# Performance work log

Measured on AMD Instinct MI355X. Metric: run time of the kernel, lower is better.

Reference implementation:

```python
import jax, jax.numpy as jnp
import numpy as np

N = 40000      # num nodes
E = 640000     # num edges (avg degree 16)
D = 128        # hidden_size
L = 2          # num_gcn


def setup_inputs() -> dict:
    key = jax.random.key(0)
    k1, k2, k3, k4, k5, k6 = jax.random.split(key, 6)
    h = jax.random.normal(k1, (N, D), dtype=jnp.float32)
    edge_src = jax.random.randint(k2, (E,), 0, N, dtype=jnp.int32)
    edge_dst = jax.random.randint(k3, (E,), 0, N, dtype=jnp.int32)
    w_self = jax.random.uniform(k4, (E,), dtype=jnp.float32)
    w_ppi = jax.random.uniform(k5, (E,), dtype=jnp.float32)
    # Xavier-uniform linear weights, zero bias (matches reset_parameters)
    limit = float(np.sqrt(6.0 / (D + D)))
    W = jax.random.uniform(k6, (L, D, D), dtype=jnp.float32, minval=-limit, maxval=limit)
    b = jnp.zeros((L, D), dtype=jnp.float32)
    return {"h": h, "edge_src": edge_src, "edge_dst": edge_dst,
            "w_self": w_self, "w_ppi": w_ppi, "W": W, "b": b}


def _agg(h, src, dst, w):
    # edge-weighted SpMM: sum over incoming edges of w_e * h[src_e]
    msgs = h[src] * w[:, None]                       # [E, D]
    return jax.ops.segment_sum(msgs, dst, num_segments=N)  # [N, D]


def reference(h, edge_src, edge_dst, w_self, w_ppi, W, b):
    for l in range(L):
        res = _agg(h, edge_src, edge_dst, w_self)        # residual aggregation
        ppi = _agg(h, edge_src, edge_dst, w_ppi)         # ppi aggregation
        # NodeUpdate: dropout(relu(linear(ppi))) + res  (dropout=0 -> identity)
        h = jax.nn.relu(ppi @ W[l].T + b[l]) + res
    return h
```

## Files before the change

### kernel.cpp

```cpp
#include <hip/hip_runtime.h>

#define D 128
#define TILE 16
#define CAP 64

typedef _Float16 f16x2 __attribute__((ext_vector_type(2)));
typedef _Float16 f16x8 __attribute__((ext_vector_type(8)));
typedef float f32x4  __attribute__((ext_vector_type(4)));

static __device__ __forceinline__ unsigned pk2h(float a, float b) {
    auto h = __builtin_amdgcn_cvt_pkrtz(a, b);
    return __builtin_bit_cast(unsigned, h);
}

__global__ __launch_bounds__(256) void cvt2z_kernel(const float4* __restrict__ a,
                                                    uint2* __restrict__ oa, int n4a,
                                                    const float4* __restrict__ bsrc,
                                                    uint2* __restrict__ ob, int n4b,
                                                    int4* __restrict__ zbuf, int nz4) {
    int i = blockIdx.x * 256 + threadIdx.x;
    if (i < n4a) {
        float4 v = a[i];
        uint2 o;
        o.x = pk2h(v.x, v.y);
        o.y = pk2h(v.z, v.w);
        oa[i] = o;
    }
    int j = i - n4a;
    if (j >= 0 && j < n4b) {
        float4 v = bsrc[j];
        uint2 o;
        o.x = pk2h(v.x, v.y);
        o.y = pk2h(v.z, v.w);
        ob[j] = o;
    }
    int k = j - n4b;
    if (k >= 0 && k < nz4) zbuf[k] = make_int4(0, 0, 0, 0);
}

__global__ __launch_bounds__(256) void build_kernel(const int* __restrict__ src,
                                                    const int* __restrict__ dst,
                                                    const float* __restrict__ wself,
                                                    const float* __restrict__ wppi,
                                                    int* __restrict__ cnt,
                                                    uint2* __restrict__ edges, int E) {
    int i = blockIdx.x * 256 + threadIdx.x;
    if (i < E) {
        int d = dst[i];
        int r = atomicAdd(&cnt[d], 1);
        if (r < CAP) {
            uint2 e;
            e.x = (unsigned)src[i];
            e.y = pk2h(wself[i], wppi[i]);
            edges[(d << 6) + r] = e;
        }
    }
}

static __device__ __forceinline__ void edge_fma(unsigned wbits, uint4 hv,
                                                f16x2 (&ra)[4], f16x2 (&pa)[4]) {
    f16x2 wv = __builtin_bit_cast(f16x2, wbits);
    f16x2 wa = {wv.x, wv.x};
    f16x2 wb = {wv.y, wv.y};
    f16x2 h01 = __builtin_bit_cast(f16x2, hv.x);
    f16x2 h23 = __builtin_bit_cast(f16x2, hv.y);
    f16x2 h45 = __builtin_bit_cast(f16x2, hv.z);
    f16x2 h67 = __builtin_bit_cast(f16x2, hv.w);
    ra[0] = __builtin_elementwise_fma(wa, h01, ra[0]);
    ra[1] = __builtin_elementwise_fma(wa, h23, ra[1]);
    ra[2] = __builtin_elementwise_fma(wa, h45, ra[2]);
    ra[3] = __builtin_elementwise_fma(wa, h67, ra[3]);
    pa[0] = __builtin_elementwise_fma(wb, h01, pa[0]);
    pa[1] = __builtin_elementwise_fma(wb, h23, pa[1]);
    pa[2] = __builtin_elementwise_fma(wb, h45, pa[2]);
    pa[3] = __builtin_elementwise_fma(wb, h67, pa[3]);
}

static __device__ __forceinline__ void agg_node(const unsigned short* __restrict__ h16,
                                                const uint2* __restrict__ edges,
                                                const uint2 (&er)[8], int cn, int beg,
                                                int q, int c8, int nn,
                                                f16x2 (&ra)[4], f16x2 (&pa)[4]) {
    int ng = (cn + 3) >> 2;
    if (ng > 8) ng = 8;
    unsigned s[8], wz[8];
    #pragma unroll
    for (int j = 0; j < 8; ++j) {
        int slot = 4 * j + q;
        bool act = slot < cn;
        unsigned sj = act ? er[j].x : er[0].x;
        s[j]  = sj < (unsigned)nn ? sj : 0u;
        wz[j] = act ? er[j].y : 0u;
    }
    uint4 hv[8];
    #pragma unroll
    for (int j = 0; j < 8; ++j)
        if (j < ng)
            hv[j] = *(const uint4*)(h16 + (size_t)s[j] * D + c8 * 8);
    #pragma unroll
    for (int j = 0; j < 8; ++j)
        if (j < ng)
            edge_fma(wz[j], hv[j], ra, pa);
    if (cn > 32) {
        int end = beg + cn;
        for (int e = beg + 32; e < end; e += 16) {
            uint2 err[4]; unsigned wzz[4];
            #pragma unroll
            for (int j = 0; j < 4; ++j) {
                int idx = e + 4 * j + q;
                bool act = idx < end;
                err[j] = edges[act ? idx : beg];
                wzz[j] = act ? err[j].y : 0u;
            }
            uint4 hh[4];
            #pragma unroll
            for (int j = 0; j < 4; ++j) {
                unsigned sj = err[j].x < (unsigned)nn ? err[j].x : 0u;
                hh[j] = *(const uint4*)(h16 + (size_t)sj * D + c8 * 8);
            }
            #pragma unroll
            for (int j = 0; j < 4; ++j) edge_fma(wzz[j], hh[j], ra, pa);
        }
    }
}

static __device__ __forceinline__ unsigned red2(unsigned x) {
    f16x2 a = __builtin_bit_cast(f16x2, x);
    unsigned u = (unsigned)__shfl_xor((int)x, 16, 64);
    a = a + __builtin_bit_cast(f16x2, u);
    unsigned u2 = (unsigned)__shfl_xor((int)__builtin_bit_cast(unsigned, a), 32, 64);
    a = a + __builtin_bit_cast(f16x2, u2);
    return __builtin_bit_cast(unsigned, a);
}

__global__ __launch_bounds__(1024, 2) void layer_kernel(const unsigned short* __restrict__ h16,
                                                        const int* __restrict__ cnt,
                                                        const uint2* __restrict__ edges,
                                                        const unsigned short* __restrict__ Wb,
                                                        const float* __restrict__ bias,
                                                        float* __restrict__ out,
                                                        unsigned short* __restrict__ out16,
                                                        int n) {
    __shared__ unsigned short ppi_lds[TILE][136];
    __shared__ float          res_lds[TILE][132];
    int t = threadIdx.x;
    int w = t >> 6, lane = t & 63;
    int tile = blockIdx.x;
    int q  = lane >> 4;
    int c8 = lane & 15;

    int m16 = lane & 15, quad = lane >> 4;
    f16x8 bfr[4] = {};
    float bb = 0.f;
    if (w < 8) {
        const _Float16* brow = (const _Float16*)Wb + (size_t)(w * 16 + m16) * D + quad * 8;
        #pragma unroll
        for (int kt = 0; kt < 4; ++kt) bfr[kt] = *(const f16x8*)(brow + kt * 32);
        bb = bias[w * 16 + m16];
    }

    int node = tile * TILE + w;
    int beg = node << 6;
    int cn = cnt[node];
    uint2 er[8];
    #pragma unroll
    for (int j = 0; j < 8; ++j) er[j] = edges[beg + 4 * j + q];

    int c = cn < CAP ? cn : CAP;
    f16x2 ra[4] = {};
    f16x2 pa[4] = {};
    agg_node(h16, edges, er, c, beg, q, c8, n, ra, pa);

    unsigned v[8];
    #pragma unroll
    for (int i = 0; i < 4; ++i) v[i]     = red2(__builtin_bit_cast(unsigned, ra[i]));
    #pragma unroll
    for (int i = 0; i < 4; ++i) v[i + 4] = red2(__builtin_bit_cast(unsigned, pa[i]));

    if (q == 0) {
        f16x2 r01 = __builtin_bit_cast(f16x2, v[0]);
        f16x2 r23 = __builtin_bit_cast(f16x2, v[1]);
        f16x2 r45 = __builtin_bit_cast(f16x2, v[2]);
        f16x2 r67 = __builtin_bit_cast(f16x2, v[3]);
        *(float4*)&res_lds[w][c8 * 8]     = make_float4((float)r01.x, (float)r01.y,
                                                        (float)r23.x, (float)r23.y);
        *(float4*)&res_lds[w][c8 * 8 + 4] = make_float4((float)r45.x, (float)r45.y,
                                                        (float)r67.x, (float)r67.y);
        uint4 o = make_uint4(v[4], v[5], v[6], v[7]);
        *(uint4*)&ppi_lds[w][c8 * 8] = o;
    }
    __syncthreads();

    if (w < 8) {
        f16x8 a[4];
        const _Float16* arow = (const _Float16*)&ppi_lds[m16][quad * 8];
        #pragma unroll
        for (int kt = 0; kt < 4; ++kt) a[kt] = *(const f16x8*)(arow + kt * 32);

        f32x4 acc = {0.f, 0.f, 0.f, 0.f};
        #pragma unroll
        for (int kt = 0; kt < 4; ++kt)
            acc = __builtin_amdgcn_mfma_f32_16x16x32_f16(a[kt], bfr[kt], acc, 0, 0, 0);

        int o = w * 16 + m16;
        #pragma unroll
        for (int r = 0; r < 4; ++r) {
            int nd = quad * 4 + r;
            float vv = fmaxf(acc[r] + bb, 0.f) + res_lds[nd][o];
            size_t gi = (size_t)(tile * TILE + nd) * D + o;
            if (out)   out[gi] = vv;
            if (out16) {
                _Float16 hvv = (_Float16)vv;
                out16[gi] = __builtin_bit_cast(unsigned short, hvv);
            }
        }
    }
}

extern "C" void kernel_launch(void* const* d_in, const int* in_sizes, int n_in,
                              void* d_out, int out_size, void* d_ws, size_t ws_size,
                              hipStream_t stream) {
    const float* h0    = (const float*)d_in[0];
    const int*   esrc  = (const int*)d_in[1];
    const int*   edst  = (const int*)d_in[2];
    const float* wself = (const float*)d_in[3];
    const float* wppi  = (const float*)d_in[4];
    const float* W     = (const float*)d_in[5];
    const float* b     = (const float*)d_in[6];
    float*       out   = (float*)d_out;

    const int N = in_sizes[0] / D;
    const int E = in_sizes[1];
    const int L = in_sizes[5] / (D * D);

    char* ws = (char*)d_ws;
    unsigned short* h16a  = (unsigned short*)ws; ws += (size_t)N * D * 2;
    unsigned short* h16b  = (unsigned short*)ws; ws += (size_t)N * D * 2;
    uint2*          edges = (uint2*)ws;          ws += (size_t)N * CAP * 8;
    unsigned short* Wb    = (unsigned short*)ws; ws += (size_t)L * D * D * 2;
    int* cnt = (int*)ws;  ws += (size_t)N * 4;

    int n4h = N * D / 4;
    int n4w = L * D * D / 4;
    int nz4 = N / 4;
    int tot = n4h + n4w + nz4;
    cvt2z_kernel<<<(tot + 255) / 256, 256, 0, stream>>>(
        (const float4*)h0, (uint2*)h16a, n4h,
        (const float4*)W, (uint2*)Wb, n4w,
        (int4*)cnt, nz4);

    int eb = (E + 255) / 256;
    build_kernel<<<eb, 256, 0, stream>>>(esrc, edst, wself, wppi, cnt, edges, E);

    int ntiles = N / TILE;
    layer_kernel<<<ntiles, 1024, 0, stream>>>(h16a, cnt, edges, Wb, b,
                                              (L > 1) ? nullptr : out,
                                              (L > 1) ? h16b : nullptr, N);
    for (int l = 1; l < L; ++l) {
        bool last = (l + 1 == L);
        layer_kernel<<<ntiles, 1024, 0, stream>>>(h16b, cnt, edges,
                                                  Wb + (size_t)l * D * D, b + (size_t)l * D,
                                                  last ? out : nullptr,
                                                  last ? nullptr : h16a, N);
        unsigned short* tmp = h16a; h16a = h16b; h16b = tmp;
    }
}
```

Before: 199.2 us.

## Halve layer block to 512 threads, two nodes per wave, zero-fill edge slots

The layer kernel now uses 512-thread blocks where each wave aggregates two nodes sequentially, so all 8 waves take part in the MFMA linear step and none sit idle. The edge bucket array is zero-filled in the conversion kernel. Padded slots then carry zero weight and src 0, which removes the per-slot masking and index clamping in the gather. The cost is an extra write of the whole edge buffer (N*64*8 bytes) on every call, traded for simpler gather code and higher occupancy.

```diff
diff --git a/kernel.cpp b/kernel.cpp
--- a/kernel.cpp
+++ b/kernel.cpp
@@ -17,7 +17,8 @@
                                                     uint2* __restrict__ oa, int n4a,
                                                     const float4* __restrict__ bsrc,
                                                     uint2* __restrict__ ob, int n4b,
-                                                    int4* __restrict__ zbuf, int nz4) {
+                                                    int4* __restrict__ z1, int nz1,
+                                                    int4* __restrict__ z2, int nz2) {
     int i = blockIdx.x * 256 + threadIdx.x;
     if (i < n4a) {
         float4 v = a[i];
@@ -35,7 +36,9 @@
         ob[j] = o;
     }
     int k = j - n4b;
-    if (k >= 0 && k < nz4) zbuf[k] = make_int4(0, 0, 0, 0);
+    if (k >= 0 && k < nz1) z1[k] = make_int4(0, 0, 0, 0);
+    int m = k - nz1;
+    if (m >= 0 && m < nz2) z2[m] = make_int4(0, 0, 0, 0);
 }
 
 __global__ __launch_bounds__(256) void build_kernel(const int* __restrict__ src,
@@ -76,54 +79,6 @@
     pa[3] = __builtin_elementwise_fma(wb, h67, pa[3]);
 }
 
-static __device__ __forceinline__ void agg_node(const unsigned short* __restrict__ h16,
-                                                const uint2* __restrict__ edges,
-                                                const uint2 (&er)[8], int cn, int beg,
-                                                int q, int c8, int nn,
-                                                f16x2 (&ra)[4], f16x2 (&pa)[4]) {
-    int ng = (cn + 3) >> 2;
-    if (ng > 8) ng = 8;
-    unsigned s[8], wz[8];
-    #pragma unroll
-    for (int j = 0; j < 8; ++j) {
-        int slot = 4 * j + q;
-        bool act = slot < cn;
-        unsigned sj = act ? er[j].x : er[0].x;
-        s[j]  = sj < (unsigned)nn ? sj : 0u;
-        wz[j] = act ? er[j].y : 0u;
-    }
-    uint4 hv[8];
-    #pragma unroll
-    for (int j = 0; j < 8; ++j)
-        if (j < ng)
-            hv[j] = *(const uint4*)(h16 + (size_t)s[j] * D + c8 * 8);
-    #pragma unroll
-    for (int j = 0; j < 8; ++j)
-        if (j < ng)
-            edge_fma(wz[j], hv[j], ra, pa);
-    if (cn > 32) {
-        int end = beg + cn;
-        for (int e = beg + 32; e < end; e += 16) {
-            uint2 err[4]; unsigned wzz[4];
-            #pragma unroll
-            for (int j = 0; j < 4; ++j) {
-                int idx = e + 4 * j + q;
-                bool act = idx < end;
-                err[j] = edges[act ? idx : beg];
-                wzz[j] = act ? err[j].y : 0u;
-            }
-            uint4 hh[4];
-            #pragma unroll
-            for (int j = 0; j < 4; ++j) {
-                unsigned sj = err[j].x < (unsigned)nn ? err[j].x : 0u;
-                hh[j] = *(const uint4*)(h16 + (size_t)sj * D + c8 * 8);
-            }
-            #pragma unroll
-            for (int j = 0; j < 4; ++j) edge_fma(wzz[j], hh[j], ra, pa);
-        }
-    }
-}
-
 static __device__ __forceinline__ unsigned red2(unsigned x) {
     f16x2 a = __builtin_bit_cast(f16x2, x);
     unsigned u = (unsigned)__shfl_xor((int)x, 16, 64);
@@ -133,14 +88,14 @@
     return __builtin_bit_cast(unsigned, a);
 }
 
-__global__ __launch_bounds__(1024, 2) void layer_kernel(const unsigned short* __restrict__ h16,
-                                                        const int* __restrict__ cnt,
-                                                        const uint2* __restrict__ edges,
-                                                        const unsigned short* __restrict__ Wb,
-                                                        const float* __restrict__ bias,
-                                                        float* __restrict__ out,
-                                                        unsigned short* __restrict__ out16,
-                                                        int n) {
+__global__ __launch_bounds__(512, 6) void layer_kernel(const unsigned short* __restrict__ h16,
+                                                       const int* __restrict__ cnt,
+                                                       const uint2* __restrict__ edges,
+                                                       const unsigned short* __restrict__ Wb,
+                                                       const float* __restrict__ bias,
+                                                       float* __restrict__ out,
+                                                       unsigned short* __restrict__ out16,
+                                                       int n) {
     __shared__ unsigned short ppi_lds[TILE][136];
     __shared__ float          res_lds[TILE][132];
     int t = threadIdx.x;
@@ -149,53 +104,75 @@
     int q  = lane >> 4;
     int c8 = lane & 15;
 
-    int m16 = lane & 15, quad = lane >> 4;
-    f16x8 bfr[4] = {};
-    float bb = 0.f;
-    if (w < 8) {
-        const _Float16* brow = (const _Float16*)Wb + (size_t)(w * 16 + m16) * D + quad * 8;
-        #pragma unroll
-        for (int kt = 0; kt < 4; ++kt) bfr[kt] = *(const f16x8*)(brow + kt * 32);
-        bb = bias[w * 16 + m16];
-    }
-
-    int node = tile * TILE + w;
-    int beg = node << 6;
-    int cn = cnt[node];
-    uint2 er[8];
     #pragma unroll
-    for (int j = 0; j < 8; ++j) er[j] = edges[beg + 4 * j + q];
-
-    int c = cn < CAP ? cn : CAP;
-    f16x2 ra[4] = {};
-    f16x2 pa[4] = {};
-    agg_node(h16, edges, er, c, beg, q, c8, n, ra, pa);
-
-    unsigned v[8];
-    #pragma unroll
-    for (int i = 0; i < 4; ++i) v[i]     = red2(__builtin_bit_cast(unsigned, ra[i]));
-    #pragma unroll
-    for (int i = 0; i < 4; ++i) v[i + 4] = red2(__builtin_bit_cast(unsigned, pa[i]));
-
-    if (q == 0) {
-        f16x2 r01 = __builtin_bit_cast(f16x2, v[0]);
-        f16x2 r23 = __builtin_bit_cast(f16x2, v[1]);
-        f16x2 r45 = __builtin_bit_cast(f16x2, v[2]);
-        f16x2 r67 = __builtin_bit_cast(f16x2, v[3]);
-        *(float4*)&res_lds[w][c8 * 8]     = make_float4((float)r01.x, (float)r01.y,
-                                                        (float)r23.x, (float)r23.y);
-        *(float4*)&res_lds[w][c8 * 8 + 4] = make_float4((float)r45.x, (float)r45.y,
-                                                        (float)r67.x, (float)r67.y);
-        uint4 o = make_uint4(v[4], v[5], v[6], v[7]);
-        *(uint4*)&ppi_lds[w][c8 * 8] = o;
+    for (int sub = 0; sub < 2; ++sub) {
+        int nd   = sub * 8 + w;
+        int node = tile * TILE + nd;
+        int beg = node << 6;
+        int cn = cnt[node];
+        int c = cn < CAP ? cn : CAP;
+        int ng = (c + 3) >> 2;
+
+        uint2 er[8];
+        #pragma unroll
+        for (int j = 0; j < 8; ++j) er[j] = edges[beg + 4 * j + q];
+
+        f16x2 ra[4] = {};
+        f16x2 pa[4] = {};
+
+        uint4 hv[8];
+        #pragma unroll
+        for (int j = 0; j < 8; ++j)
+            if (j < ng)
+                hv[j] = *(const uint4*)(h16 + (size_t)er[j].x * D + c8 * 8);
+        #pragma unroll
+        for (int j = 0; j < 8; ++j)
+            if (j < ng)
+                edge_fma(er[j].y, hv[j], ra, pa);
+
+        if (ng > 8) {
+            for (int j = 8; j < 16; ++j) {
+                if (j < ng) {
+                    uint2 e2 = edges[beg + 4 * j + q];
+                    uint4 hh = *(const uint4*)(h16 + (size_t)e2.x * D + c8 * 8);
+                    edge_fma(e2.y, hh, ra, pa);
+                }
+            }
+        }
+
+        unsigned v[8];
+        #pragma unroll
+        for (int i = 0; i < 4; ++i) v[i]     = red2(__builtin_bit_cast(unsigned, ra[i]));
+        #pragma unroll
+        for (int i = 0; i < 4; ++i) v[i + 4] = red2(__builtin_bit_cast(unsigned, pa[i]));
+
+        if (q == 0) {
+            f16x2 r01 = __builtin_bit_cast(f16x2, v[0]);
+            f16x2 r23 = __builtin_bit_cast(f16x2, v[1]);
+            f16x2 r45 = __builtin_bit_cast(f16x2, v[2]);
+            f16x2 r67 = __builtin_bit_cast(f16x2, v[3]);
+            *(float4*)&res_lds[nd][c8 * 8]     = make_float4((float)r01.x, (float)r01.y,
+                                                             (float)r23.x, (float)r23.y);
+            *(float4*)&res_lds[nd][c8 * 8 + 4] = make_float4((float)r45.x, (float)r45.y,
+                                                             (float)r67.x, (float)r67.y);
+            uint4 o = make_uint4(v[4], v[5], v[6], v[7]);
+            *(uint4*)&ppi_lds[nd][c8 * 8] = o;
+        }
     }
     __syncthreads();
 
-    if (w < 8) {
+    {
+        int m16 = lane & 15, quad = lane >> 4;
         f16x8 a[4];
         const _Float16* arow = (const _Float16*)&ppi_lds[m16][quad * 8];
         #pragma unroll
         for (int kt = 0; kt < 4; ++kt) a[kt] = *(const f16x8*)(arow + kt * 32);
+
+        f16x8 bfr[4];
+        const _Float16* brow = (const _Float16*)Wb + (size_t)(w * 16 + m16) * D + quad * 8;
+        #pragma unroll
+        for (int kt = 0; kt < 4; ++kt) bfr[kt] = *(const f16x8*)(brow + kt * 32);
+        float bb = bias[w * 16 + m16];
 
         f32x4 acc = {0.f, 0.f, 0.f, 0.f};
         #pragma unroll
@@ -242,26 +219,28 @@
 
     int n4h = N * D / 4;
     int n4w = L * D * D / 4;
-    int nz4 = N / 4;
-    int tot = n4h + n4w + nz4;
+    int nz1 = N * CAP / 2;
+    int nz2 = N / 4;
+    int tot = n4h + n4w + nz1 + nz2;
     cvt2z_kernel<<<(tot + 255) / 256, 256, 0, stream>>>(
         (const float4*)h0, (uint2*)h16a, n4h,
         (const float4*)W, (uint2*)Wb, n4w,
-        (int4*)cnt, nz4);
+        (int4*)edges, nz1,
+        (int4*)cnt, nz2);
 
     int eb = (E + 255) / 256;
     build_kernel<<<eb, 256, 0, stream>>>(esrc, edst, wself, wppi, cnt, edges, E);
 
     int ntiles = N / TILE;
-    layer_kernel<<<ntiles, 1024, 0, stream>>>(h16a, cnt, edges, Wb, b,
-                                              (L > 1) ? nullptr : out,
-                                              (L > 1) ? h16b : nullptr, N);
+    layer_kernel<<<ntiles, 512, 0, stream>>>(h16a, cnt, edges, Wb, b,
+                                             (L > 1) ? nullptr : out,
+                                             (L > 1) ? h16b : nullptr, N);
     for (int l = 1; l < L; ++l) {
         bool last = (l + 1 == L);
-        layer_kernel<<<ntiles, 1024, 0, stream>>>(h16b, cnt, edges,
-                                                  Wb + (size_t)l * D * D, b + (size_t)l * D,
-                                                  last ? out : nullptr,
-                                                  last ? nullptr : h16a, N);
+        layer_kernel<<<ntiles, 512, 0, stream>>>(h16b, cnt, edges,
+                                                 Wb + (size_t)l * D * D, b + (size_t)l * D,
+                                                 last ? out : nullptr,
+                                                 last ? nullptr : h16a, N);
         unsigned short* tmp = h16a; h16a = h16b; h16b = tmp;
     }
 }
```

Result: faster. 181.5 us (-8.9%).
